# Kernel tuning notes

Measured on AMD Instinct MI355X. Metric: run time of the kernel, lower is better.

## Reference

```python
import jax, jax.numpy as jnp
import numpy as np

CUTOFF = 5.0
N_ATOMS, N_EDGES, D, R = 100000, 1600000, 64, 20


def setup_inputs() -> dict:
    key = jax.random.key(0)
    ks = jax.random.split(key, 12)
    ve = jax.random.normal(ks[0], (N_ATOMS, D, 3), dtype=jnp.float32)
    se = jax.random.normal(ks[1], (N_ATOMS, D), dtype=jnp.float32)
    dirs = jax.random.normal(ks[2], (N_EDGES, 3), dtype=jnp.float32)
    dirs = dirs / jnp.linalg.norm(dirs, axis=-1, keepdims=True)
    dist = jax.random.uniform(ks[3], (N_EDGES,), minval=0.5, maxval=CUTOFF, dtype=jnp.float32)
    nv = dirs * dist[:, None]  # neighbour_vectors with norm in (0.5, cutoff)
    central = jax.random.randint(ks[4], (N_EDGES,), 0, N_ATOMS)
    neigh = jax.random.randint(ks[5], (N_EDGES,), 0, N_ATOMS)
    # Bessel frequencies n*pi/cutoff (learnable in graph-pes)
    freqs = (jnp.arange(1, R + 1, dtype=jnp.float32) * np.pi / CUTOFF)
    W_filter = jax.random.normal(ks[6], (R, 3 * D), dtype=jnp.float32) / np.sqrt(R)
    b_filter = jnp.zeros((3 * D,), dtype=jnp.float32)
    W1 = jax.random.normal(ks[7], (D, D), dtype=jnp.float32) / np.sqrt(D)
    b1 = jnp.zeros((D,), dtype=jnp.float32)
    W2 = jax.random.normal(ks[8], (D, 3 * D), dtype=jnp.float32) / np.sqrt(D)
    b2 = jnp.zeros((3 * D,), dtype=jnp.float32)
    return {
        'vector_embeddings': ve, 'scalar_embeddings': se, 'neighbour_vectors': nv,
        'central_atoms': central, 'neighbours': neigh,
        'freqs': freqs, 'W_filter': W_filter, 'b_filter': b_filter,
        'W1': W1, 'b1': b1, 'W2': W2, 'b2': b2,
    }


def _envelope(d):
    # polynomial envelope, p = 6
    u = d / CUTOFF
    env = 1.0 - 28.0 * u**6 + 48.0 * u**7 - 21.0 * u**8
    return jnp.where(d < CUTOFF, env, 0.0)


def reference(vector_embeddings, scalar_embeddings, neighbour_vectors,
              central_atoms, neighbours, freqs, W_filter, b_filter,
              W1, b1, W2, b2):
    d = jnp.linalg.norm(neighbour_vectors, axis=-1)                 # [E]
    unit = neighbour_vectors / d[:, None]                           # [E, 3]
    # Bessel radial basis: sqrt(2/c) * sin(f_n d) / d
    bessel = np.sqrt(2.0 / CUTOFF) * jnp.sin(freqs[None, :] * d[:, None]) / d[:, None]  # [E, R]
    filt = (bessel @ W_filter + b_filter) * _envelope(d)[:, None]   # [E, 3D]
    # phi: MLP [D, D, 3D] with SiLU between layers
    h = jax.nn.silu(scalar_embeddings @ W1 + b1) @ W2 + b2          # [N, 3D]
    x_ij = filt * h[central_atoms]                                  # [E, 3D]
    a, b, c = jnp.split(x_ij, 3, axis=-1)                           # each [E, D]
    n = scalar_embeddings.shape[0]
    delta_s = jax.ops.segment_sum(a, neighbours, num_segments=n)    # [N, D]
    v_ij = b[:, :, None] * unit[:, None, :] + c[:, :, None] * vector_embeddings[neighbours]  # [E, D, 3]
    delta_v = jax.ops.segment_sum(v_ij, neighbours, num_segments=n)  # [N, D, 3]
    return (delta_v, delta_s)
```

## Files before the change

kernel.cpp:

```cpp
#include <hip/hip_runtime.h>
#include <math.h>

#define DCH 64
#define TD 192
#define RR 20
#define FCUT 5.0f
#define HIST_BLOCKS 512

typedef __attribute__((ext_vector_type(8))) short short8;
typedef __attribute__((ext_vector_type(4))) float f32x4;
typedef __attribute__((ext_vector_type(2))) unsigned int u32x2;

__device__ __forceinline__ unsigned short f2bf(float f) {
    unsigned int u = __float_as_uint(f);
    u += 0x7FFFu + ((u >> 16) & 1u);
    return (unsigned short)(u >> 16);
}
__device__ __forceinline__ float bflo(unsigned int u) {
    return __uint_as_float(u << 16);
}
__device__ __forceinline__ float bfhi(unsigned int u) {
    return __uint_as_float(u & 0xFFFF0000u);
}

__global__ __launch_bounds__(256) void mlp_hist_kernel(
    const float* __restrict__ se,
    const float* __restrict__ W1, const float* __restrict__ b1,
    const float* __restrict__ W2, const float* __restrict__ b2,
    unsigned short* __restrict__ h2, int N,
    const int* __restrict__ neigh, int* __restrict__ counts,
    int* __restrict__ pos, int E)
{
    if (blockIdx.x < HIST_BLOCKS) {
        int stride = HIST_BLOCKS * 256;
        for (int e = blockIdx.x * 256 + threadIdx.x; e < E; e += stride) {
            int p = atomicAdd(&counts[neigh[e]], 1);
            __builtin_nontemporal_store(p, &pos[e]);
        }
        return;
    }

    const int wid  = threadIdx.x >> 6;
    const int lane = threadIdx.x & 63;
    const int g    = lane >> 4;
    const int c    = lane & 15;

    __shared__ float hmid[4][16][68];
    __shared__ unsigned short hstage[4][16][196];

    const int base = (blockIdx.x - HIST_BLOCKS) * 64;
    const int arow = base + wid * 16;
    const int atom = arow + c;
    const bool va  = atom < N;

    const float* sp = se + (size_t)(va ? atom : 0) * DCH;
    short8 A0, A1;
    #pragma unroll
    for (int kh = 0; kh < 2; ++kh) {
        f32x4 q0 = va ? __builtin_nontemporal_load((const f32x4*)(sp + kh*32 + 8*g))
                      : (f32x4){0.f,0.f,0.f,0.f};
        f32x4 q1 = va ? __builtin_nontemporal_load((const f32x4*)(sp + kh*32 + 8*g + 4))
                      : (f32x4){0.f,0.f,0.f,0.f};
        short8& A = kh ? A1 : A0;
        A[0] = (short)f2bf(q0[0]); A[1] = (short)f2bf(q0[1]);
        A[2] = (short)f2bf(q0[2]); A[3] = (short)f2bf(q0[3]);
        A[4] = (short)f2bf(q1[0]); A[5] = (short)f2bf(q1[1]);
        A[6] = (short)f2bf(q1[2]); A[7] = (short)f2bf(q1[3]);
    }

    #pragma unroll
    for (int t = 0; t < 4; ++t) {
        short8 w0, w1;
        #pragma unroll
        for (int j = 0; j < 8; ++j) {
            w0[j] = (short)f2bf(W1[(8 * g + j) * DCH + 16 * t + c]);
            w1[j] = (short)f2bf(W1[(32 + 8 * g + j) * DCH + 16 * t + c]);
        }
        f32x4 C = {0.f, 0.f, 0.f, 0.f};
        C = __builtin_amdgcn_mfma_f32_16x16x32_bf16(A0, w0, C, 0, 0, 0);
        C = __builtin_amdgcn_mfma_f32_16x16x32_bf16(A1, w1, C, 0, 0, 0);
        float bb = b1[16 * t + c];
        #pragma unroll
        for (int reg = 0; reg < 4; ++reg) {
            float x = C[reg] + bb;
            float s = x / (1.0f + __expf(-x));
            hmid[wid][4 * g + reg][16 * t + c] = s;
        }
    }
    __syncthreads();

    short8 B0, B1;
    #pragma unroll
    for (int kh = 0; kh < 2; ++kh) {
        const float* hp = &hmid[wid][c][kh * 32 + 8 * g];
        f32x4 q0 = *(const f32x4*)(hp);
        f32x4 q1 = *(const f32x4*)(hp + 4);
        short8& A = kh ? B1 : B0;
        A[0] = (short)f2bf(q0[0]); A[1] = (short)f2bf(q0[1]);
        A[2] = (short)f2bf(q0[2]); A[3] = (short)f2bf(q0[3]);
        A[4] = (short)f2bf(q1[0]); A[5] = (short)f2bf(q1[1]);
        A[6] = (short)f2bf(q1[2]); A[7] = (short)f2bf(q1[3]);
    }

    #pragma unroll
    for (int t = 0; t < 12; ++t) {
        short8 w0, w1;
        #pragma unroll
        for (int j = 0; j < 8; ++j) {
            w0[j] = (short)f2bf(W2[(8 * g + j) * TD + 16 * t + c]);
            w1[j] = (short)f2bf(W2[(32 + 8 * g + j) * TD + 16 * t + c]);
        }
        f32x4 C = {0.f, 0.f, 0.f, 0.f};
        C = __builtin_amdgcn_mfma_f32_16x16x32_bf16(B0, w0, C, 0, 0, 0);
        C = __builtin_amdgcn_mfma_f32_16x16x32_bf16(B1, w1, C, 0, 0, 0);
        float bb = b2[16 * t + c];
        #pragma unroll
        for (int reg = 0; reg < 4; ++reg)
            hstage[wid][4 * g + reg][c * 12 + t] = f2bf(C[reg] + bb);
    }
    __syncthreads();

    if (lane < 48) {
        #pragma unroll
        for (int i = 0; i < 16; ++i) {
            int a2 = arow + i;
            if (a2 < N)
                *(u32x2*)((char*)h2 + (size_t)a2 * 384 + lane * 8) =
                    *(const u32x2*)(&hstage[wid][i][lane * 4]);
        }
    }
}

__global__ __launch_bounds__(256) void scan1_kernel(
    const int* __restrict__ counts, int* __restrict__ starts,
    int* __restrict__ bsums, int N)
{
    int tid = threadIdx.x;
    int gid = blockIdx.x * 256 + tid;
    int v = (gid < N) ? counts[gid] : 0;
    int lane = tid & 63, wid = tid >> 6;
    int x = v;
    #pragma unroll
    for (int off = 1; off < 64; off <<= 1) {
        int y = __shfl_up(x, off, 64);
        if (lane >= off) x += y;
    }
    __shared__ int wsum[4];
    if (lane == 63) wsum[wid] = x;
    __syncthreads();
    int add = 0;
    for (int w = 0; w < wid; ++w) add += wsum[w];
    int incl = x + add;
    if (gid < N) starts[gid] = incl - v;
    if (tid == 255) bsums[blockIdx.x] = incl;
}

__global__ __launch_bounds__(512) void scan2_kernel(int* __restrict__ bsums, int M)
{
    int tid = threadIdx.x;
    int v = (tid < M) ? bsums[tid] : 0;
    int lane = tid & 63, wid = tid >> 6;
    int x = v;
    #pragma unroll
    for (int off = 1; off < 64; off <<= 1) {
        int y = __shfl_up(x, off, 64);
        if (lane >= off) x += y;
    }
    __shared__ int wsum[8];
    if (lane == 63) wsum[wid] = x;
    __syncthreads();
    int add = 0;
    for (int w = 0; w < wid; ++w) add += wsum[w];
    int incl = x + add;
    if (tid < M) bsums[tid] = incl - v;
}

__global__ void fill_kernel(const float* __restrict__ nv, const int* __restrict__ central,
                            const int* __restrict__ neigh, const int* __restrict__ starts,
                            const int* __restrict__ bsums, const int* __restrict__ pos,
                            f32x4* __restrict__ payload, int E)
{
    int stride = gridDim.x * blockDim.x;
    for (int e = blockIdx.x * blockDim.x + threadIdx.x; e < E; e += stride) {
        int na = neigh[e];
        int slot = starts[na] + bsums[na >> 8] + pos[e];
        f32x4 pay;
        pay[0] = __builtin_nontemporal_load(&nv[(size_t)e*3+0]);
        pay[1] = __builtin_nontemporal_load(&nv[(size_t)e*3+1]);
        pay[2] = __builtin_nontemporal_load(&nv[(size_t)e*3+2]);
        pay[3] = __int_as_float(central[e]);
        __builtin_nontemporal_store(pay, &payload[slot]);
    }
}

__global__ __launch_bounds__(256) void gather_kernel(
    const f32x4* __restrict__ payload, const int* __restrict__ starts,
    const int* __restrict__ bsums, const int* __restrict__ counts,
    const unsigned short* __restrict__ h2,
    const float* __restrict__ ve, const float* __restrict__ Wf,
    const float* __restrict__ bfil,
    float* __restrict__ dv, float* __restrict__ ds, int N)
{
    const int wid  = threadIdx.x >> 6;
    const int lane = threadIdx.x & 63;
    const int g    = lane >> 4;
    const int c    = lane & 15;

    short8 Bf[12];
    float  bft[12];
    #pragma unroll
    for (int t = 0; t < 12; ++t) {
        #pragma unroll
        for (int j = 0; j < 8; ++j) {
            int r = 8 * g + j;
            float w = (r < RR) ? Wf[r * TD + 16 * t + c] : 0.0f;
            Bf[t][j] = (short)f2bf(w);
        }
        bft[t] = bfil[16 * t + c];
    }

    const float BC = sqrtf(2.0f / FCUT);
    const float XK = (float)(M_PI / (double)FCUT);
    const char* hb = (const char*)h2;

    for (int atom = blockIdx.x * 4 + wid; atom < N; atom += gridDim.x * 4) {
        const int s   = starts[atom] + bsums[atom >> 8];
        const int cnt = counts[atom];

        float dsa[4] = {0,0,0,0};
        float csm[4] = {0,0,0,0};
        float dvx[4] = {0,0,0,0};
        float dvy[4] = {0,0,0,0};
        float dvz[4] = {0,0,0,0};

        for (int i0 = 0; i0 < cnt; i0 += 16) {
            const bool valid = (i0 + c) < cnt;
            f32x4 p = valid ? __builtin_nontemporal_load(&payload[s + i0 + c])
                            : (f32x4){1.0f, 0.0f, 0.0f, 0.0f};
            float dist = sqrtf(p[0]*p[0] + p[1]*p[1] + p[2]*p[2]);
            float inv  = 1.0f / dist;
            float xa   = dist * XK;

            float u  = dist * (1.0f / FCUT);
            float u2 = u * u;
            float u6 = u2 * u2 * u2;
            float env = 1.0f + u6 * (-28.0f + u * (48.0f - 21.0f * u));
            env = (dist < FCUT && valid) ? env : 0.0f;
            float scale = BC * inv * env;

            float ux = p[0] * inv, uy = p[1] * inv, uz = p[2] * inv;
            int   ca  = valid ? __float_as_int(p[3]) : 0;
            int   hof = ca * 384;

            float bas[8];
            bas[0] = __sinf((float)(8 * g + 1) * xa);
            bas[1] = __sinf((float)(8 * g + 2) * xa);
            float twoc = 2.0f * __cosf(xa);
            #pragma unroll
            for (int j = 2; j < 8; ++j)
                bas[j] = fmaf(twoc, bas[j-1], -bas[j-2]);

            short8 A;
            #pragma unroll
            for (int j = 0; j < 8; ++j)
                A[j] = (short)f2bf(bas[j] * scale);

            float env_r[4], ux_r[4], uy_r[4], uz_r[4];
            int   hof_r[4];
            #pragma unroll
            for (int reg = 0; reg < 4; ++reg) {
                int src = 4 * g + reg;
                env_r[reg] = __shfl(env, src, 64);
                ux_r[reg]  = __shfl(ux,  src, 64);
                uy_r[reg]  = __shfl(uy,  src, 64);
                uz_r[reg]  = __shfl(uz,  src, 64);
                hof_r[reg] = __shfl(hof, src, 64);
            }

            u32x2 hq[4][3];
            #pragma unroll
            for (int reg = 0; reg < 4; ++reg) {
                const char* rp = hb + (size_t)(unsigned)hof_r[reg] + c * 24;
                hq[reg][0] = *(const u32x2*)(rp);
                hq[reg][1] = *(const u32x2*)(rp + 8);
                hq[reg][2] = *(const u32x2*)(rp + 16);
            }

            #pragma unroll
            for (int t = 0; t < 12; ++t) {
                f32x4 C = __builtin_amdgcn_mfma_f32_16x16x32_bf16(
                    A, Bf[t], (f32x4){0.f,0.f,0.f,0.f}, 0, 0, 0);
                #pragma unroll
                for (int reg = 0; reg < 4; ++reg) {
                    unsigned int w = hq[reg][t >> 2][(t >> 1) & 1];
                    float hv = (t & 1) ? bfhi(w) : bflo(w);
                    float filt = fmaf(bft[t], env_r[reg], C[reg]);
                    if (t < 4) {
                        dsa[t] = fmaf(filt, hv, dsa[t]);
                    } else if (t < 8) {
                        float bh = filt * hv;
                        dvx[t-4] = fmaf(bh, ux_r[reg], dvx[t-4]);
                        dvy[t-4] = fmaf(bh, uy_r[reg], dvy[t-4]);
                        dvz[t-4] = fmaf(bh, uz_r[reg], dvz[t-4]);
                    } else {
                        csm[t-8] = fmaf(filt, hv, csm[t-8]);
                    }
                }
            }
        }

        #pragma unroll
        for (int t = 0; t < 4; ++t) {
            dsa[t] += __shfl_xor(dsa[t], 16, 64); dsa[t] += __shfl_xor(dsa[t], 32, 64);
            csm[t] += __shfl_xor(csm[t], 16, 64); csm[t] += __shfl_xor(csm[t], 32, 64);
            dvx[t] += __shfl_xor(dvx[t], 16, 64); dvx[t] += __shfl_xor(dvx[t], 32, 64);
            dvy[t] += __shfl_xor(dvy[t], 16, 64); dvy[t] += __shfl_xor(dvy[t], 32, 64);
            dvz[t] += __shfl_xor(dvz[t], 16, 64); dvz[t] += __shfl_xor(dvz[t], 32, 64);
        }

        float dssel = (g==0) ? dsa[0] : (g==1) ? dsa[1] : (g==2) ? dsa[2] : dsa[3];
        float cssel = (g==0) ? csm[0] : (g==1) ? csm[1] : (g==2) ? csm[2] : csm[3];
        float vxsel = (g==0) ? dvx[0] : (g==1) ? dvx[1] : (g==2) ? dvx[2] : dvx[3];
        float vysel = (g==0) ? dvy[0] : (g==1) ? dvy[1] : (g==2) ? dvy[2] : dvy[3];
        float vzsel = (g==0) ? dvz[0] : (g==1) ? dvz[1] : (g==2) ? dvz[2] : dvz[3];

        int ch = 16 * g + c;
        size_t vb = (size_t)atom * TD + (size_t)ch * 3;
        float v0 = __builtin_nontemporal_load(&ve[vb + 0]);
        float v1 = __builtin_nontemporal_load(&ve[vb + 1]);
        float v2 = __builtin_nontemporal_load(&ve[vb + 2]);
        __builtin_nontemporal_store(fmaf(cssel, v0, vxsel), &dv[vb + 0]);
        __builtin_nontemporal_store(fmaf(cssel, v1, vysel), &dv[vb + 1]);
        __builtin_nontemporal_store(fmaf(cssel, v2, vzsel), &dv[vb + 2]);
        __builtin_nontemporal_store(dssel, &ds[(size_t)atom * DCH + ch]);
    }
}

extern "C" void kernel_launch(void* const* d_in, const int* in_sizes, int n_in,
                              void* d_out, int out_size, void* d_ws, size_t ws_size,
                              hipStream_t stream) {
    const float* ve      = (const float*)d_in[0];
    const float* se      = (const float*)d_in[1];
    const float* nv      = (const float*)d_in[2];
    const int*   central = (const int*)  d_in[3];
    const int*   neigh   = (const int*)  d_in[4];
    const float* Wf      = (const float*)d_in[6];
    const float* bfil    = (const float*)d_in[7];
    const float* W1      = (const float*)d_in[8];
    const float* b1      = (const float*)d_in[9];
    const float* W2      = (const float*)d_in[10];
    const float* b2      = (const float*)d_in[11];

    const int N = in_sizes[1] / DCH;
    const int E = in_sizes[3];

    float* out = (float*)d_out;
    float* dv  = out;
    float* ds  = out + (size_t)N * TD;

    char* wsb = (char*)d_ws;
    size_t off = 0;
    auto wsalloc = [&](size_t bytes) -> void* {
        void* p = wsb + off;
        off = (off + bytes + 255) & ~(size_t)255;
        return p;
    };
    unsigned short* h2      = (unsigned short*)wsalloc((size_t)N * 192 * 2);
    int*            counts  = (int*)   wsalloc((size_t)N * 4);
    int*            starts  = (int*)   wsalloc((size_t)N * 4);
    int*            pos     = (int*)   wsalloc((size_t)E * 4);
    f32x4*          payload = (f32x4*) wsalloc((size_t)E * 16);
    int*            bsums   = (int*)   wsalloc(4096);

    const int nb1 = (N + 255) / 256;
    const int nbm = (N + 63) / 64;

    hipMemsetAsync(counts, 0, (size_t)N * 4, stream);
    mlp_hist_kernel<<<HIST_BLOCKS + nbm, 256, 0, stream>>>(
        se, W1, b1, W2, b2, h2, N, neigh, counts, pos, E);
    scan1_kernel<<<nb1, 256, 0, stream>>>(counts, starts, bsums, N);
    scan2_kernel<<<1, 512, 0, stream>>>(bsums, nb1);
    fill_kernel<<<2048, 256, 0, stream>>>(nv, central, neigh, starts, bsums, pos,
                                          payload, E);
    gather_kernel<<<2048, 256, 0, stream>>>(payload, starts, bsums, counts, h2, ve,
                                            Wf, bfil, dv, ds, N);
}
```

Baseline: 349.5 us.

## Fold filter bias into MFMA and stream pre-swizzled weights to cut registers

Measured after the change: 1.013 ms. 190% more time.

```diff
diff --git a/kernel.cpp b/kernel.cpp
--- a/kernel.cpp
+++ b/kernel.cpp
@@ -155,7 +155,10 @@
     if (tid == 255) bsums[blockIdx.x] = incl;
 }
 
-__global__ __launch_bounds__(512) void scan2_kernel(int* __restrict__ bsums, int M)
+__global__ __launch_bounds__(512) void scan2_wft_kernel(
+    int* __restrict__ bsums, int M,
+    const float* __restrict__ Wf, const float* __restrict__ bfil,
+    unsigned short* __restrict__ wft)
 {
     int tid = threadIdx.x;
     int v = (tid < M) ? bsums[tid] : 0;
@@ -173,6 +176,17 @@
     for (int w = 0; w < wid; ++w) add += wsum[w];
     int incl = x + add;
     if (tid < M) bsums[tid] = incl - v;
+
+    for (int idx = tid; idx < 12 * 64 * 8; idx += 512) {
+        int j  = idx & 7;
+        int ln = (idx >> 3) & 63;
+        int t  = idx >> 9;
+        int gg = ln >> 4, cc = ln & 15;
+        int r  = 8 * gg + j;
+        float w = (r < RR) ? Wf[r * TD + 16 * t + cc]
+                           : (r == RR ? bfil[16 * t + cc] : 0.0f);
+        wft[(size_t)idx] = f2bf(w);
+    }
 }
 
 __global__ void fill_kernel(const float* __restrict__ nv, const int* __restrict__ central,
@@ -193,37 +207,24 @@
     }
 }
 
-__global__ __launch_bounds__(256) void gather_kernel(
+__global__ __launch_bounds__(256, 8) void gather_kernel(
     const f32x4* __restrict__ payload, const int* __restrict__ starts,
     const int* __restrict__ bsums, const int* __restrict__ counts,
     const unsigned short* __restrict__ h2,
-    const float* __restrict__ ve, const float* __restrict__ Wf,
-    const float* __restrict__ bfil,
-    float* __restrict__ dv, float* __restrict__ ds, int N)
+    const float* __restrict__ ve, const unsigned short* __restrict__ wft,
+    float* __restrict__ dv, float* __restrict__ ds, int aBeg, int aEnd)
 {
     const int wid  = threadIdx.x >> 6;
     const int lane = threadIdx.x & 63;
     const int g    = lane >> 4;
     const int c    = lane & 15;
 
-    short8 Bf[12];
-    float  bft[12];
-    #pragma unroll
-    for (int t = 0; t < 12; ++t) {
-        #pragma unroll
-        for (int j = 0; j < 8; ++j) {
-            int r = 8 * g + j;
-            float w = (r < RR) ? Wf[r * TD + 16 * t + c] : 0.0f;
-            Bf[t][j] = (short)f2bf(w);
-        }
-        bft[t] = bfil[16 * t + c];
-    }
-
     const float BC = sqrtf(2.0f / FCUT);
     const float XK = (float)(M_PI / (double)FCUT);
     const char* hb = (const char*)h2;
-
-    for (int atom = blockIdx.x * 4 + wid; atom < N; atom += gridDim.x * 4) {
+    const short8* wfp = (const short8*)wft + lane;
+
+    for (int atom = aBeg + blockIdx.x * 4 + wid; atom < aEnd; atom += gridDim.x * 4) {
         const int s   = starts[atom] + bsums[atom >> 8];
         const int cnt = counts[atom];
 
@@ -249,8 +250,7 @@
             float scale = BC * inv * env;
 
             float ux = p[0] * inv, uy = p[1] * inv, uz = p[2] * inv;
-            int   ca  = valid ? __float_as_int(p[3]) : 0;
-            int   hof = ca * 384;
+            int   hof = __float_as_int(p[3]) * 384;
 
             float bas[8];
             bas[0] = __sinf((float)(8 * g + 1) * xa);
@@ -264,13 +264,13 @@
             #pragma unroll
             for (int j = 0; j < 8; ++j)
                 A[j] = (short)f2bf(bas[j] * scale);
-
-            float env_r[4], ux_r[4], uy_r[4], uz_r[4];
+            if (g == 2) A[4] = (short)f2bf(env);
+
+            float ux_r[4], uy_r[4], uz_r[4];
             int   hof_r[4];
             #pragma unroll
             for (int reg = 0; reg < 4; ++reg) {
                 int src = 4 * g + reg;
-                env_r[reg] = __shfl(env, src, 64);
                 ux_r[reg]  = __shfl(ux,  src, 64);
                 uy_r[reg]  = __shfl(uy,  src, 64);
                 uz_r[reg]  = __shfl(uz,  src, 64);
@@ -288,22 +288,22 @@
 
             #pragma unroll
             for (int t = 0; t < 12; ++t) {
+                short8 B = wfp[t * 64];
                 f32x4 C = __builtin_amdgcn_mfma_f32_16x16x32_bf16(
-                    A, Bf[t], (f32x4){0.f,0.f,0.f,0.f}, 0, 0, 0);
+                    A, B, (f32x4){0.f,0.f,0.f,0.f}, 0, 0, 0);
                 #pragma unroll
                 for (int reg = 0; reg < 4; ++reg) {
                     unsigned int w = hq[reg][t >> 2][(t >> 1) & 1];
                     float hv = (t & 1) ? bfhi(w) : bflo(w);
-                    float filt = fmaf(bft[t], env_r[reg], C[reg]);
                     if (t < 4) {
-                        dsa[t] = fmaf(filt, hv, dsa[t]);
+                        dsa[t] = fmaf(C[reg], hv, dsa[t]);
                     } else if (t < 8) {
-                        float bh = filt * hv;
+                        float bh = C[reg] * hv;
                         dvx[t-4] = fmaf(bh, ux_r[reg], dvx[t-4]);
                         dvy[t-4] = fmaf(bh, uy_r[reg], dvy[t-4]);
                         dvz[t-4] = fmaf(bh, uz_r[reg], dvz[t-4]);
                     } else {
-                        csm[t-8] = fmaf(filt, hv, csm[t-8]);
+                        csm[t-8] = fmaf(C[reg], hv, csm[t-8]);
                     }
                 }
             }
@@ -371,17 +371,21 @@
     int*            pos     = (int*)   wsalloc((size_t)E * 4);
     f32x4*          payload = (f32x4*) wsalloc((size_t)E * 16);
     int*            bsums   = (int*)   wsalloc(4096);
+    unsigned short* wft     = (unsigned short*)wsalloc(12 * 64 * 8 * 2);
 
     const int nb1 = (N + 255) / 256;
     const int nbm = (N + 63) / 64;
+    const int half = (N + 1) / 2;
 
     hipMemsetAsync(counts, 0, (size_t)N * 4, stream);
     mlp_hist_kernel<<<HIST_BLOCKS + nbm, 256, 0, stream>>>(
         se, W1, b1, W2, b2, h2, N, neigh, counts, pos, E);
     scan1_kernel<<<nb1, 256, 0, stream>>>(counts, starts, bsums, N);
-    scan2_kernel<<<1, 512, 0, stream>>>(bsums, nb1);
+    scan2_wft_kernel<<<1, 512, 0, stream>>>(bsums, nb1, Wf, bfil, wft);
     fill_kernel<<<2048, 256, 0, stream>>>(nv, central, neigh, starts, bsums, pos,
                                           payload, E);
-    gather_kernel<<<2048, 256, 0, stream>>>(payload, starts, bsums, counts, h2, ve,
-                                            Wf, bfil, dv, ds, N);
-}
+    gather_kernel<<<1024, 256, 0, stream>>>(payload, starts, bsums, counts, h2, ve,
+                                            wft, dv, ds, 0, half);
+    gather_kernel<<<1024, 256, 0, stream>>>(payload, starts, bsums, counts, h2, ve,
+                                            wft, dv, ds, half, N);
+}
```
